# Performance work log

Hardware: AMD Instinct MI355X
Metric: run time of the kernel (lower is better)

The kernel has to match this reference:

```python
import jax, jax.numpy as jnp
import numpy as np

DIM = 1024
N_HEADS = 16
D_HEAD = DIM // N_HEADS


def setup_inputs() -> dict:
    key = jax.random.key(0)
    ks = jax.random.split(key, 7)
    s = DIM ** -0.5
    return {
        "x": jax.random.normal(ks[0], (4, 2048, DIM), dtype=jnp.float32),
        "Wq": jax.random.normal(ks[1], (DIM, DIM), dtype=jnp.float32) * s,
        "bq": jax.random.normal(ks[2], (DIM,), dtype=jnp.float32) * 0.02,
        "Wk": jax.random.normal(ks[3], (DIM, DIM), dtype=jnp.float32) * s,
        "bk": jax.random.normal(ks[4], (DIM,), dtype=jnp.float32) * 0.02,
        "Wv": jax.random.normal(ks[5], (DIM, DIM), dtype=jnp.float32) * s,
        "bv": jax.random.normal(ks[6], (DIM,), dtype=jnp.float32) * 0.02,
    }


def reference(x, Wq, bq, Wk, bk, Wv, bv):
    B, N, D = x.shape
    H, Dh = N_HEADS, D_HEAD

    def split_heads(t):
        # b n (h d) -> b h n d
        return t.reshape(B, N, H, Dh).transpose(0, 2, 1, 3)

    q = split_heads(x @ Wq + bq)
    k = split_heads(x @ Wk + bk)
    v = split_heads(x @ Wv + bv)

    scale = Dh ** -0.5
    logit = jnp.einsum("bhnd,bhmd->bhnm", q, k) * scale  # [B,H,N,N]
    attn = jax.nn.softmax(logit, axis=-1)
    out = jnp.einsum("bhnm,bhmd->bhnd", attn, v)
    # b h n d -> b n (h d)
    return out.transpose(0, 2, 1, 3).reshape(B, N, D)
```

## Files before the change

### kernel.cpp

```cpp
#include <hip/hip_runtime.h>
#include <hip/hip_bf16.h>
#include <stdint.h>

#define BB 4
#define SEQ 2048
#define DIM 1024
#define NH 16
#define DH 64
#define MM (BB*SEQ)

typedef unsigned short u16;
typedef __attribute__((ext_vector_type(8))) __bf16 bf16x8;
typedef __attribute__((ext_vector_type(4))) float floatx4;
typedef __attribute__((ext_vector_type(4))) unsigned short u16x4;

#define QSCALE 0.18033688011112042f

__device__ __forceinline__ u16 f2bf(float f) {
    union { float f; unsigned u; } v; v.f = f;
    unsigned u = v.u;
    u += 0x7FFF + ((u >> 16) & 1);
    return (u16)(u >> 16);
}

__device__ __forceinline__ bf16x8 ldb8(const u16* p) {
    return *(const bf16x8*)(const void*)p;
}

__device__ __forceinline__ void async_copy16(const u16* g, u16* l) {
    __builtin_amdgcn_global_load_lds(
        (const __attribute__((address_space(1))) unsigned int*)g,
        (__attribute__((address_space(3))) unsigned int*)l, 16, 0, 0);
}

__global__ __launch_bounds__(256)
void conv_x(const float* __restrict__ x, u16* __restrict__ xb) {
    const size_t i = ((size_t)blockIdx.x * 256 + threadIdx.x) * 4;
    float4 f = *(const float4*)(x + i);
    u16x4 o = { f2bf(f.x), f2bf(f.y), f2bf(f.z), f2bf(f.w) };
    *(u16x4*)(xb + i) = o;
}

__global__ __launch_bounds__(256)
void conv_wt(const float* __restrict__ Wq, const float* __restrict__ Wk,
             const float* __restrict__ Wv, u16* __restrict__ Wt) {
    const int t = blockIdx.z;
    const float* W = (t == 0) ? Wq : (t == 1) ? Wk : Wv;
    u16* D = Wt + (size_t)t * DIM * DIM;
    __shared__ u16 T[64][65];
    const int k0 = blockIdx.x * 64, n0 = blockIdx.y * 64;
    const int tid = threadIdx.x;
    #pragma unroll
    for (int p = 0; p < 4; p++) {
        const int r = p * 16 + (tid >> 4), c = (tid & 15) * 4;
        float4 f = *(const float4*)(W + (size_t)(k0 + r) * DIM + n0 + c);
        T[c + 0][r] = f2bf(f.x); T[c + 1][r] = f2bf(f.y);
        T[c + 2][r] = f2bf(f.z); T[c + 3][r] = f2bf(f.w);
    }
    __syncthreads();
    #pragma unroll
    for (int p = 0; p < 4; p++) {
        const int rn = p * 16 + (tid >> 4), ck = (tid & 15) * 4;
        u16x4 v = { T[rn][ck], T[rn][ck + 1], T[rn][ck + 2], T[rn][ck + 3] };
        *(u16x4*)(D + (size_t)(n0 + rn) * DIM + k0 + ck) = v;
    }
}

__global__ __launch_bounds__(256)
void qkv_gemm2(const u16* __restrict__ xb, const u16* __restrict__ Wt,
               const float* __restrict__ bq, const float* __restrict__ bk,
               const float* __restrict__ bv, u16* __restrict__ ws) {
    __shared__ u16 As[128 * 32];
    __shared__ u16 Bs[128 * 32];

    const int m0 = blockIdx.x * 128;
    const int t  = blockIdx.y >> 3;
    const int c0 = (blockIdx.y & 7) * 128;
    const u16* Wtb = Wt + (size_t)t * DIM * DIM;
    const float* bias = (t == 0) ? bq : (t == 1) ? bk : bv;
    const float osc = (t == 0) ? QSCALE : 1.0f;
    u16* dst = ws + (size_t)t * ((size_t)MM * DIM);

    const int tid  = threadIdx.x;
    const int lane = tid & 63;
    const int w    = tid >> 6;
    const int wr = w >> 1, wc = w & 1;
    const int g = lane >> 4, ln = lane & 15;

    floatx4 acc[4][4];
    #pragma unroll
    for (int i = 0; i < 4; i++)
        #pragma unroll
        for (int j = 0; j < 4; j++) acc[i][j] = (floatx4){0.f,0.f,0.f,0.f};

    const int srow = w * 16 + (lane >> 2);
    const int skof = (lane & 3) * 8;

    for (int kk = 0; kk < DIM; kk += 32) {
        const u16* ga0 = xb  + (size_t)(m0 + srow)      * DIM + kk + skof;
        const u16* ga1 = xb  + (size_t)(m0 + 64 + srow) * DIM + kk + skof;
        const u16* gb0 = Wtb + (size_t)(c0 + srow)      * DIM + kk + skof;
        const u16* gb1 = Wtb + (size_t)(c0 + 64 + srow) * DIM + kk + skof;
        async_copy16(ga0, &As[w * 512]);
        async_copy16(ga1, &As[2048 + w * 512]);
        async_copy16(gb0, &Bs[w * 512]);
        async_copy16(gb1, &Bs[2048 + w * 512]);
        __syncthreads();

        bf16x8 a[4], b[4];
        #pragma unroll
        for (int fr = 0; fr < 4; fr++)
            a[fr] = ldb8(&As[(wr*64 + fr*16 + ln) * 32 + g*8]);
        #pragma unroll
        for (int fc = 0; fc < 4; fc++)
            b[fc] = ldb8(&Bs[(wc*64 + fc*16 + ln) * 32 + g*8]);

        #pragma unroll
        for (int fr = 0; fr < 4; fr++)
            #pragma unroll
            for (int fc = 0; fc < 4; fc++)
                acc[fr][fc] = __builtin_amdgcn_mfma_f32_16x16x32_bf16(
                    a[fr], b[fc], acc[fr][fc], 0, 0, 0);
        __syncthreads();
    }

    #pragma unroll
    for (int fc = 0; fc < 4; fc++) {
        const int cc = c0 + wc*64 + fc*16 + ln;
        const float bias_v = bias[cc];
        const int h = cc >> 6, d = cc & 63;
        #pragma unroll
        for (int fr = 0; fr < 4; fr++) {
            const int mrow = m0 + wr*64 + fr*16 + g*4;
            const int bidx = mrow >> 11, nn = mrow & 2047;
            if (t < 2) {
                #pragma unroll
                for (int rr = 0; rr < 4; rr++)
                    dst[((size_t)(bidx*NH + h)*SEQ + nn + rr)*DH + d] =
                        f2bf((acc[fr][fc][rr] + bias_v) * osc);
            } else {
                u16x4 v = { f2bf(acc[fr][fc][0] + bias_v), f2bf(acc[fr][fc][1] + bias_v),
                            f2bf(acc[fr][fc][2] + bias_v), f2bf(acc[fr][fc][3] + bias_v) };
                *(u16x4*)&dst[((size_t)(bidx*NH + h)*DH + d)*SEQ + nn] = v;
            }
        }
    }
}

#define LDA 40
__global__ __launch_bounds__(256)
void qkv_gemm(const float* __restrict__ x,
              const float* __restrict__ Wq, const float* __restrict__ bq,
              const float* __restrict__ Wk, const float* __restrict__ bk,
              const float* __restrict__ Wv, const float* __restrict__ bv,
              u16* __restrict__ ws) {
    __shared__ u16 As[128 * LDA];
    __shared__ u16 Bs[128 * LDA];
    const int m0 = blockIdx.x * 128;
    const int t  = blockIdx.y >> 3;
    const int c0 = (blockIdx.y & 7) * 128;
    const float* W    = (t == 0) ? Wq : (t == 1) ? Wk : Wv;
    const float* bias = (t == 0) ? bq : (t == 1) ? bk : bv;
    const float osc = (t == 0) ? QSCALE : 1.0f;
    u16* dst = ws + (size_t)t * ((size_t)MM * DIM);
    const int tid  = threadIdx.x;
    const int lane = tid & 63;
    const int wave = tid >> 6;
    const int wr = wave >> 1, wc = wave & 1;
    const int g = lane >> 4, ln = lane & 15;
    floatx4 acc[4][4];
    #pragma unroll
    for (int i = 0; i < 4; i++)
        #pragma unroll
        for (int j = 0; j < 4; j++) acc[i][j] = (floatx4){0.f,0.f,0.f,0.f};
    const int ar  = tid >> 1;
    const int ak  = (tid & 1) * 16;
    const int bkr = tid & 31;
    const int bc  = (tid >> 5) * 16;
    for (int kk = 0; kk < DIM; kk += 32) {
        {
            const float4* s4 = (const float4*)(x + (size_t)(m0 + ar) * DIM + kk + ak);
            float4 f0 = s4[0], f1 = s4[1], f2 = s4[2], f3 = s4[3];
            unsigned pk[8];
            pk[0] = f2bf(f0.x) | ((unsigned)f2bf(f0.y) << 16);
            pk[1] = f2bf(f0.z) | ((unsigned)f2bf(f0.w) << 16);
            pk[2] = f2bf(f1.x) | ((unsigned)f2bf(f1.y) << 16);
            pk[3] = f2bf(f1.z) | ((unsigned)f2bf(f1.w) << 16);
            pk[4] = f2bf(f2.x) | ((unsigned)f2bf(f2.y) << 16);
            pk[5] = f2bf(f2.z) | ((unsigned)f2bf(f2.w) << 16);
            pk[6] = f2bf(f3.x) | ((unsigned)f2bf(f3.y) << 16);
            pk[7] = f2bf(f3.z) | ((unsigned)f2bf(f3.w) << 16);
            uint4* d = (uint4*)&As[ar * LDA + ak];
            d[0] = make_uint4(pk[0], pk[1], pk[2], pk[3]);
            d[1] = make_uint4(pk[4], pk[5], pk[6], pk[7]);
        }
        {
            const float4* s4 = (const float4*)(W + (size_t)(kk + bkr) * DIM + c0 + bc);
            float4 f0 = s4[0], f1 = s4[1], f2 = s4[2], f3 = s4[3];
            float fv[16] = {f0.x,f0.y,f0.z,f0.w, f1.x,f1.y,f1.z,f1.w,
                            f2.x,f2.y,f2.z,f2.w, f3.x,f3.y,f3.z,f3.w};
            #pragma unroll
            for (int j = 0; j < 16; j++)
                Bs[(bc + j) * LDA + bkr] = f2bf(fv[j]);
        }
        __syncthreads();
        bf16x8 a[4], b[4];
        #pragma unroll
        for (int fr = 0; fr < 4; fr++)
            a[fr] = ldb8(&As[(wr*64 + fr*16 + ln) * LDA + g*8]);
        #pragma unroll
        for (int fc = 0; fc < 4; fc++)
            b[fc] = ldb8(&Bs[(wc*64 + fc*16 + ln) * LDA + g*8]);
        #pragma unroll
        for (int fr = 0; fr < 4; fr++)
            #pragma unroll
            for (int fc = 0; fc < 4; fc++)
                acc[fr][fc] = __builtin_amdgcn_mfma_f32_16x16x32_bf16(
                    a[fr], b[fc], acc[fr][fc], 0, 0, 0);
        __syncthreads();
    }
    #pragma unroll
    for (int fc = 0; fc < 4; fc++) {
        const int cc = c0 + wc*64 + fc*16 + ln;
        const float bias_v = bias[cc];
        const int h = cc >> 6, d = cc & 63;
        #pragma unroll
        for (int fr = 0; fr < 4; fr++) {
            #pragma unroll
            for (int rr = 0; rr < 4; rr++) {
                const int mrow = m0 + wr*64 + fr*16 + g*4 + rr;
                const int bidx = mrow >> 11, nn = mrow & 2047;
                const float val = (acc[fr][fc][rr] + bias_v) * osc;
                size_t idx;
                if (t < 2) idx = ((size_t)(bidx*NH + h)*SEQ + nn)*DH + d;
                else       idx = ((size_t)(bidx*NH + h)*DH + d)*SEQ + nn;
                dst[idx] = f2bf(val);
            }
        }
    }
}

#define LDP 72

__global__ __launch_bounds__(256, 3)
void attn4(const u16* __restrict__ ws, float* __restrict__ out) {
    const int qt = blockIdx.x;
    const int h  = blockIdx.y;
    const int b  = blockIdx.z;
    const int bh = b*NH + h;

    const u16* Qw = ws;
    const u16* Kw = ws + (size_t)MM * DIM;
    const u16* Vt = ws + 2 * (size_t)MM * DIM;

    __shared__ u16 Kbuf[2][4096];
    __shared__ u16 Vbuf[2][4096];
    __shared__ u16 P[4][32 * LDP];

    const int tid  = threadIdx.x;
    const int lane = tid & 63;
    const int w    = tid >> 6;
    const int g = lane >> 4, ln = lane & 15;
    const int q0 = qt*128 + w*32;

    const int srow = w*8 + (lane >> 3);
    const int sseg = (lane & 7) ^ ((lane >> 3) & 7);
    const u16* kg = Kw + ((size_t)bh*SEQ + srow)*DH + sseg*8;
    const u16* vg = Vt + ((size_t)bh*DH + srow)*SEQ + sseg*8;

    const int fs0 = ((0*4 + g) ^ (ln & 7)) * 8;
    const int fs1 = ((1*4 + g) ^ (ln & 7)) * 8;

    bf16x8 aq[2][2];
    #pragma unroll
    for (int rb = 0; rb < 2; rb++) {
        const u16* qp = Qw + ((size_t)bh*SEQ + q0 + rb*16 + ln)*DH + g*8;
        aq[rb][0] = ldb8(qp);
        aq[rb][1] = ldb8(qp + 32);
    }

    floatx4 acc[2][4];
    #pragma unroll
    for (int rb = 0; rb < 2; rb++)
        #pragma unroll
        for (int i = 0; i < 4; i++) acc[rb][i] = (floatx4){0.f,0.f,0.f,0.f};
    float lrun[2] = {0.f, 0.f};

    u16* Pw = &P[w][0];

    {
        async_copy16(kg,                  &Kbuf[0][w*512]);
        async_copy16(kg + (size_t)32*DH,  &Kbuf[0][2048 + w*512]);
        async_copy16(vg,                  &Vbuf[0][w*512]);
        async_copy16(vg + (size_t)32*SEQ, &Vbuf[0][2048 + w*512]);
    }
    __syncthreads();

    for (int kt = 0; kt < 32; kt++) {
        const int cur = kt & 1;
        if (kt < 31) {
            const int nxt = cur ^ 1;
            const size_t ko = (size_t)(kt + 1) * 64 * DH;
            const size_t vo = (size_t)(kt + 1) * 64;
            async_copy16(kg + ko,                  &Kbuf[nxt][w*512]);
            async_copy16(kg + ko + (size_t)32*DH,  &Kbuf[nxt][2048 + w*512]);
            async_copy16(vg + vo,                  &Vbuf[nxt][w*512]);
            async_copy16(vg + vo + (size_t)32*SEQ, &Vbuf[nxt][2048 + w*512]);
        }

        const u16* Kc = &Kbuf[cur][0];
        const u16* Vc = &Vbuf[cur][0];

        bf16x8 bkf[4][2];
        #pragma unroll
        for (int fn = 0; fn < 4; fn++) {
            bkf[fn][0] = ldb8(&Kc[(fn*16 + ln)*64 + fs0]);
            bkf[fn][1] = ldb8(&Kc[(fn*16 + ln)*64 + fs1]);
        }
        bf16x8 av[4][2];
        #pragma unroll
        for (int fd = 0; fd < 4; fd++) {
            av[fd][0] = ldb8(&Vc[(fd*16 + ln)*64 + fs0]);
            av[fd][1] = ldb8(&Vc[(fd*16 + ln)*64 + fs1]);
        }

        #pragma unroll
        for (int rb = 0; rb < 2; rb++) {
            #pragma unroll
            for (int fn = 0; fn < 4; fn++) {
                floatx4 z = (floatx4){0.f,0.f,0.f,0.f};
                z = __builtin_amdgcn_mfma_f32_16x16x32_bf16(bkf[fn][0], aq[rb][0], z, 0, 0, 0);
                z = __builtin_amdgcn_mfma_f32_16x16x32_bf16(bkf[fn][1], aq[rb][1], z, 0, 0, 0);
                float p0 = __builtin_amdgcn_exp2f(z[0]);
                float p1 = __builtin_amdgcn_exp2f(z[1]);
                float p2 = __builtin_amdgcn_exp2f(z[2]);
                float p3 = __builtin_amdgcn_exp2f(z[3]);
                lrun[rb] += (p0 + p1) + (p2 + p3);
                __hip_bfloat162 lo = __float22bfloat162_rn(make_float2(p0, p1));
                __hip_bfloat162 hi = __float22bfloat162_rn(make_float2(p2, p3));
                union { __hip_bfloat162 v2[2]; u16x4 v4; } u;
                u.v2[0] = lo; u.v2[1] = hi;
                *(u16x4*)&Pw[(rb*16 + ln)*LDP + fn*16 + g*4] = u.v4;
            }
        }

        bf16x8 bp[2][2];
        #pragma unroll
        for (int rb = 0; rb < 2; rb++) {
            bp[rb][0] = ldb8(&Pw[(rb*16 + ln)*LDP + g*8]);
            bp[rb][1] = ldb8(&Pw[(rb*16 + ln)*LDP + 32 + g*8]);
        }

        #pragma unroll
        for (int fd = 0; fd < 4; fd++)
            #pragma unroll
            for (int rb = 0; rb < 2; rb++) {
                acc[rb][fd] = __builtin_amdgcn_mfma_f32_16x16x32_bf16(av[fd][0], bp[rb][0], acc[rb][fd], 0, 0, 0);
                acc[rb][fd] = __builtin_amdgcn_mfma_f32_16x16x32_bf16(av[fd][1], bp[rb][1], acc[rb][fd], 0, 0, 0);
            }

        __syncthreads();
    }

    #pragma unroll
    for (int rb = 0; rb < 2; rb++) {
        float v = lrun[rb];
        v += __shfl_xor(v, 16, 64);
        v += __shfl_xor(v, 32, 64);
        lrun[rb] = v;
    }
    #pragma unroll
    for (int rb = 0; rb < 2; rb++) {
        const float inv = 1.0f / lrun[rb];
        const int n = q0 + rb*16 + ln;
        #pragma unroll
        for (int fd = 0; fd < 4; fd++) {
            floatx4 v = acc[rb][fd];
            float4 o = { v[0]*inv, v[1]*inv, v[2]*inv, v[3]*inv };
            *(float4*)&out[((size_t)b*SEQ + n)*DIM + h*DH + fd*16 + g*4] = o;
        }
    }
}

extern "C" void kernel_launch(void* const* d_in, const int* in_sizes, int n_in,
                              void* d_out, int out_size, void* d_ws, size_t ws_size,
                              hipStream_t stream) {
    const float* x  = (const float*)d_in[0];
    const float* Wq = (const float*)d_in[1];
    const float* bq = (const float*)d_in[2];
    const float* Wk = (const float*)d_in[3];
    const float* bk = (const float*)d_in[4];
    const float* Wv = (const float*)d_in[5];
    const float* bv = (const float*)d_in[6];
    u16* ws = (u16*)d_ws;
    float* out = (float*)d_out;

    const size_t need = (size_t)4 * MM * DIM * 2 + (size_t)3 * DIM * DIM * 2;
    if (ws_size >= need) {
        u16* xb = ws + (size_t)3 * MM * DIM;
        u16* Wt = ws + (size_t)4 * MM * DIM;
        conv_x<<<dim3(MM*DIM/1024), 256, 0, stream>>>(x, xb);
        conv_wt<<<dim3(DIM/64, DIM/64, 3), 256, 0, stream>>>(Wq, Wk, Wv, Wt);
        qkv_gemm2<<<dim3(MM/128, 24), 256, 0, stream>>>(xb, Wt, bq, bk, bv, ws);
    } else {
        qkv_gemm<<<dim3(MM/128, 24), 256, 0, stream>>>(x, Wq, bq, Wk, bk, Wv, bv, ws);
    }
    attn4<<<dim3(SEQ/128, NH, BB), 256, 0, stream>>>(ws, out);
}
```

Before: 275.6 us.

## Double attention query rows per wave and vectorize Q/K GEMM epilogue stores

The attention kernel now processes 64 query rows per wave (256 per block), so each K/V tile loaded into shared memory is reused across twice as many queries. This halves the grid and K/V global traffic but raises register pressure, so the launch-bounds occupancy hint drops from 3 to 2. V fragment loads are moved after the QK/softmax phase to shorten their live range. The QKV GEMM swaps MFMA operand order for Q and K so the accumulator layout allows 4-wide bf16 stores and float4 bias loads in the epilogue.

```diff
diff --git a/kernel.cpp b/kernel.cpp
--- a/kernel.cpp
+++ b/kernel.cpp
@@ -115,30 +115,51 @@
         for (int fc = 0; fc < 4; fc++)
             b[fc] = ldb8(&Bs[(wc*64 + fc*16 + ln) * 32 + g*8]);
 
-        #pragma unroll
-        for (int fr = 0; fr < 4; fr++)
-            #pragma unroll
-            for (int fc = 0; fc < 4; fc++)
-                acc[fr][fc] = __builtin_amdgcn_mfma_f32_16x16x32_bf16(
-                    a[fr], b[fc], acc[fr][fc], 0, 0, 0);
+        if (t < 2) {
+            #pragma unroll
+            for (int fr = 0; fr < 4; fr++)
+                #pragma unroll
+                for (int fc = 0; fc < 4; fc++)
+                    acc[fr][fc] = __builtin_amdgcn_mfma_f32_16x16x32_bf16(
+                        b[fc], a[fr], acc[fr][fc], 0, 0, 0);
+        } else {
+            #pragma unroll
+            for (int fr = 0; fr < 4; fr++)
+                #pragma unroll
+                for (int fc = 0; fc < 4; fc++)
+                    acc[fr][fc] = __builtin_amdgcn_mfma_f32_16x16x32_bf16(
+                        a[fr], b[fc], acc[fr][fc], 0, 0, 0);
+        }
         __syncthreads();
     }
 
-    #pragma unroll
-    for (int fc = 0; fc < 4; fc++) {
-        const int cc = c0 + wc*64 + fc*16 + ln;
-        const float bias_v = bias[cc];
-        const int h = cc >> 6, d = cc & 63;
-        #pragma unroll
-        for (int fr = 0; fr < 4; fr++) {
-            const int mrow = m0 + wr*64 + fr*16 + g*4;
-            const int bidx = mrow >> 11, nn = mrow & 2047;
-            if (t < 2) {
-                #pragma unroll
-                for (int rr = 0; rr < 4; rr++)
-                    dst[((size_t)(bidx*NH + h)*SEQ + nn + rr)*DH + d] =
-                        f2bf((acc[fr][fc][rr] + bias_v) * osc);
-            } else {
+    if (t < 2) {
+        #pragma unroll
+        for (int fc = 0; fc < 4; fc++) {
+            const int cc = c0 + wc*64 + fc*16 + g*4;
+            const float4 b4 = *(const float4*)&bias[cc];
+            const int h = cc >> 6, d = cc & 63;
+            #pragma unroll
+            for (int fr = 0; fr < 4; fr++) {
+                const int tok = m0 + wr*64 + fr*16 + ln;
+                const int bidx = tok >> 11, nn = tok & 2047;
+                u16x4 v = { f2bf((acc[fr][fc][0] + b4.x) * osc),
+                            f2bf((acc[fr][fc][1] + b4.y) * osc),
+                            f2bf((acc[fr][fc][2] + b4.z) * osc),
+                            f2bf((acc[fr][fc][3] + b4.w) * osc) };
+                *(u16x4*)&dst[((size_t)(bidx*NH + h)*SEQ + nn)*DH + d] = v;
+            }
+        }
+    } else {
+        #pragma unroll
+        for (int fc = 0; fc < 4; fc++) {
+            const int cc = c0 + wc*64 + fc*16 + ln;
+            const float bias_v = bias[cc];
+            const int h = cc >> 6, d = cc & 63;
+            #pragma unroll
+            for (int fr = 0; fr < 4; fr++) {
+                const int mrow = m0 + wr*64 + fr*16 + g*4;
+                const int bidx = mrow >> 11, nn = mrow & 2047;
                 u16x4 v = { f2bf(acc[fr][fc][0] + bias_v), f2bf(acc[fr][fc][1] + bias_v),
                             f2bf(acc[fr][fc][2] + bias_v), f2bf(acc[fr][fc][3] + bias_v) };
                 *(u16x4*)&dst[((size_t)(bidx*NH + h)*DH + d)*SEQ + nn] = v;
@@ -242,8 +263,8 @@
 
 #define LDP 72
 
-__global__ __launch_bounds__(256, 3)
-void attn4(const u16* __restrict__ ws, float* __restrict__ out) {
+__global__ __launch_bounds__(256, 2)
+void attn5(const u16* __restrict__ ws, float* __restrict__ out) {
     const int qt = blockIdx.x;
     const int h  = blockIdx.y;
     const int b  = blockIdx.z;
@@ -255,13 +276,13 @@
 
     __shared__ u16 Kbuf[2][4096];
     __shared__ u16 Vbuf[2][4096];
-    __shared__ u16 P[4][32 * LDP];
+    __shared__ u16 P[4][64 * LDP];
 
     const int tid  = threadIdx.x;
     const int lane = tid & 63;
     const int w    = tid >> 6;
     const int g = lane >> 4, ln = lane & 15;
-    const int q0 = qt*128 + w*32;
+    const int q0 = qt*256 + w*64;
 
     const int srow = w*8 + (lane >> 3);
     const int sseg = (lane & 7) ^ ((lane >> 3) & 7);
@@ -271,29 +292,27 @@
     const int fs0 = ((0*4 + g) ^ (ln & 7)) * 8;
     const int fs1 = ((1*4 + g) ^ (ln & 7)) * 8;
 
-    bf16x8 aq[2][2];
-    #pragma unroll
-    for (int rb = 0; rb < 2; rb++) {
+    bf16x8 aq[4][2];
+    #pragma unroll
+    for (int rb = 0; rb < 4; rb++) {
         const u16* qp = Qw + ((size_t)bh*SEQ + q0 + rb*16 + ln)*DH + g*8;
         aq[rb][0] = ldb8(qp);
         aq[rb][1] = ldb8(qp + 32);
     }
 
-    floatx4 acc[2][4];
-    #pragma unroll
-    for (int rb = 0; rb < 2; rb++)
+    floatx4 acc[4][4];
+    #pragma unroll
+    for (int rb = 0; rb < 4; rb++)
         #pragma unroll
         for (int i = 0; i < 4; i++) acc[rb][i] = (floatx4){0.f,0.f,0.f,0.f};
-    float lrun[2] = {0.f, 0.f};
+    float lrun[4] = {0.f, 0.f, 0.f, 0.f};
 
     u16* Pw = &P[w][0];
 
-    {
-        async_copy16(kg,                  &Kbuf[0][w*512]);
-        async_copy16(kg + (size_t)32*DH,  &Kbuf[0][2048 + w*512]);
-        async_copy16(vg,                  &Vbuf[0][w*512]);
-        async_copy16(vg + (size_t)32*SEQ, &Vbuf[0][2048 + w*512]);
-    }
+    async_copy16(kg,                  &Kbuf[0][w*512]);
+    async_copy16(kg + (size_t)32*DH,  &Kbuf[0][2048 + w*512]);
+    async_copy16(vg,                  &Vbuf[0][w*512]);
+    async_copy16(vg + (size_t)32*SEQ, &Vbuf[0][2048 + w*512]);
     __syncthreads();
 
     for (int kt = 0; kt < 32; kt++) {
@@ -317,15 +336,9 @@
             bkf[fn][0] = ldb8(&Kc[(fn*16 + ln)*64 + fs0]);
             bkf[fn][1] = ldb8(&Kc[(fn*16 + ln)*64 + fs1]);
         }
-        bf16x8 av[4][2];
-        #pragma unroll
-        for (int fd = 0; fd < 4; fd++) {
-            av[fd][0] = ldb8(&Vc[(fd*16 + ln)*64 + fs0]);
-            av[fd][1] = ldb8(&Vc[(fd*16 + ln)*64 + fs1]);
-        }
-
-        #pragma unroll
-        for (int rb = 0; rb < 2; rb++) {
+
+        #pragma unroll
+        for (int rb = 0; rb < 4; rb++) {
             #pragma unroll
             for (int fn = 0; fn < 4; fn++) {
                 floatx4 z = (floatx4){0.f,0.f,0.f,0.f};
@@ -344,9 +357,15 @@
             }
         }
 
-        bf16x8 bp[2][2];
-        #pragma unroll
-        for (int rb = 0; rb < 2; rb++) {
+        bf16x8 av[4][2];
+        #pragma unroll
+        for (int fd = 0; fd < 4; fd++) {
+            av[fd][0] = ldb8(&Vc[(fd*16 + ln)*64 + fs0]);
+            av[fd][1] = ldb8(&Vc[(fd*16 + ln)*64 + fs1]);
+        }
+        bf16x8 bp[4][2];
+        #pragma unroll
+        for (int rb = 0; rb < 4; rb++) {
             bp[rb][0] = ldb8(&Pw[(rb*16 + ln)*LDP + g*8]);
             bp[rb][1] = ldb8(&Pw[(rb*16 + ln)*LDP + 32 + g*8]);
         }
@@ -354,7 +373,7 @@
         #pragma unroll
         for (int fd = 0; fd < 4; fd++)
             #pragma unroll
-            for (int rb = 0; rb < 2; rb++) {
+            for (int rb = 0; rb < 4; rb++) {
                 acc[rb][fd] = __builtin_amdgcn_mfma_f32_16x16x32_bf16(av[fd][0], bp[rb][0], acc[rb][fd], 0, 0, 0);
                 acc[rb][fd] = __builtin_amdgcn_mfma_f32_16x16x32_bf16(av[fd][1], bp[rb][1], acc[rb][fd], 0, 0, 0);
             }
@@ -363,14 +382,14 @@
     }
 
     #pragma unroll
-    for (int rb = 0; rb < 2; rb++) {
+    for (int rb = 0; rb < 4; rb++) {
         float v = lrun[rb];
         v += __shfl_xor(v, 16, 64);
         v += __shfl_xor(v, 32, 64);
         lrun[rb] = v;
     }
     #pragma unroll
-    for (int rb = 0; rb < 2; rb++) {
+    for (int rb = 0; rb < 4; rb++) {
         const float inv = 1.0f / lrun[rb];
         const int n = q0 + rb*16 + ln;
         #pragma unroll
@@ -405,5 +424,5 @@
     } else {
         qkv_gemm<<<dim3(MM/128, 24), 256, 0, stream>>>(x, Wq, bq, Wk, bk, Wv, bv, ws);
     }
-    attn4<<<dim3(SEQ/128, NH, BB), 256, 0, stream>>>(ws, out);
-}
+    attn5<<<dim3(SEQ/256, NH, BB), 256, 0, stream>>>(ws, out);
+}
```

Measured after the change: 259.4 us. 5.9% less time.
